# Optimization experiments

Hardware: AMD Instinct MI355X
Metric: run time of the kernel (lower is better)

## Reference

```python
import jax, jax.numpy as jnp
import numpy as np

PS = 8; STRIDE = 4; KNN = 8; POOL_RATIO = 0.5; NHEADS = 4
EPS_BN = 1e-5; EPS_LN = 1e-5


def _conv(x, w, b):
    y = jax.lax.conv_general_dilated(x, w, (1, 1), ((1, 1), (1, 1)),
                                     dimension_numbers=('NCHW', 'OIHW', 'NCHW'))
    return y + b[None, :, None, None]


def _bn_eval(x, g, b):
    # BatchNorm2d in eval mode with running_mean=0, running_var=1
    return x * (g / np.sqrt(1.0 + EPS_BN))[None, :, None, None] + b[None, :, None, None]


def _maxpool2(x):
    return jax.lax.reduce_window(x, -jnp.inf, jax.lax.max, (1, 1, 2, 2), (1, 1, 2, 2), 'VALID')


def _layernorm(x, g, b):
    m = jnp.mean(x, axis=-1, keepdims=True)
    v = jnp.var(x, axis=-1, keepdims=True)
    return (x - m) / jnp.sqrt(v + EPS_LN) * g + b


def _mha(x, in_w, in_b, out_w, out_b):
    # batched self-attention, x: (B,S,E); matches nn.MultiheadAttention eval
    B, S, E = x.shape
    hd = E // NHEADS
    qkv = x @ in_w.T + in_b                      # (B,S,3E)
    q, k, v = jnp.split(qkv, 3, axis=-1)
    def heads(t):
        return t.reshape(B, S, NHEADS, hd).transpose(0, 2, 1, 3)
    q, k, v = heads(q), heads(k), heads(v)
    att = jax.nn.softmax(jnp.einsum('bhqd,bhkd->bhqk', q, k) / np.sqrt(hd), axis=-1)
    o = jnp.einsum('bhqk,bhkd->bhqd', att, v).transpose(0, 2, 1, 3).reshape(B, S, E)
    return o @ out_w.T + out_b


def _extract_patches(feat):
    # F.unfold(feat, kernel=PS, stride=STRIDE) -> (B, N, C*PS*PS), flat order (c, ki, kj)
    B, C, H, W = feat.shape
    nph = (H - PS) // STRIDE + 1
    npw = (W - PS) // STRIDE + 1
    hi = STRIDE * jnp.arange(nph)[:, None] + jnp.arange(PS)   # (nph, PS)
    wi = STRIDE * jnp.arange(npw)[:, None] + jnp.arange(PS)   # (npw, PS)
    p = feat[:, :, hi]            # (B,C,nph,PS,W)
    p = p[:, :, :, :, wi]         # (B,C,nph,PS,npw,PS)
    p = p.transpose(0, 2, 4, 1, 3, 5).reshape(B, nph * npw, C * PS * PS)
    return p, nph, npw


def _adjacency(nph, npw):
    # positions form a deterministic grid, identical across the batch -> static adjacency
    ii, jj = np.meshgrid(np.arange(nph), np.arange(npw), indexing='ij')
    pos = np.stack([ii.ravel(), jj.ravel()], axis=1).astype(np.float32)  # (N,2)
    N = pos.shape[0]
    d = np.linalg.norm(pos[:, None, :] - pos[None, :, :], axis=-1)
    order = np.argsort(d, axis=1, kind='stable')          # ascending; col 0 is self
    tgt = order[:, 1:KNN + 1]                             # (N, KNN)
    src = np.repeat(np.arange(N), KNN)
    adj = np.zeros((N, N), dtype=np.float32)
    adj[src, tgt.ravel()] = 1.0
    adj2 = ((adj @ adj) > 0).astype(np.float32)
    np.fill_diagonal(adj2, 0.0)
    return jnp.asarray(adj), jnp.asarray(adj2)


def setup_inputs() -> dict:
    key = jax.random.key(0)
    ks = jax.random.split(key, 16)
    def lin(k, o, i):
        return jax.random.normal(k, (o, i), jnp.float32) / np.sqrt(float(i))
    B = 16
    inp = {}
    inp['x'] = jax.random.normal(ks[0], (B, 3, 256, 256), jnp.float32)
    inp['conv1_w'] = jax.random.normal(ks[1], (64, 3, 3, 3), jnp.float32) / np.sqrt(27.0)
    inp['conv1_b'] = jnp.zeros((64,), jnp.float32)
    inp['bn1_g'] = jnp.ones((64,), jnp.float32); inp['bn1_b'] = jnp.zeros((64,), jnp.float32)
    inp['conv2_w'] = jax.random.normal(ks[2], (64, 64, 3, 3), jnp.float32) / np.sqrt(576.0)
    inp['conv2_b'] = jnp.zeros((64,), jnp.float32)
    inp['bn2_g'] = jnp.ones((64,), jnp.float32); inp['bn2_b'] = jnp.zeros((64,), jnp.float32)
    inp['proj_w'] = lin(ks[3], 128, 4096); inp['proj_b'] = jnp.zeros((128,), jnp.float32)
    inp['w1_w'] = lin(ks[4], 128, 128); inp['w1_b'] = jnp.zeros((128,), jnp.float32)
    inp['w2_w'] = lin(ks[5], 128, 128); inp['w2_b'] = jnp.zeros((128,), jnp.float32)
    inp['gate_w'] = lin(ks[6], 128, 256); inp['gate_b'] = jnp.zeros((128,), jnp.float32)
    inp['score_w'] = lin(ks[7], 1, 128); inp['score_b'] = jnp.zeros((1,), jnp.float32)
    inp['in_proj_w'] = lin(ks[8], 384, 128); inp['in_proj_b'] = jnp.zeros((384,), jnp.float32)
    inp['out_proj_w'] = lin(ks[9], 128, 128); inp['out_proj_b'] = jnp.zeros((128,), jnp.float32)
    inp['ff1_w'] = lin(ks[10], 512, 128); inp['ff1_b'] = jnp.zeros((512,), jnp.float32)
    inp['ff2_w'] = lin(ks[11], 128, 512); inp['ff2_b'] = jnp.zeros((128,), jnp.float32)
    inp['ln1_g'] = jnp.ones((128,), jnp.float32); inp['ln1_b'] = jnp.zeros((128,), jnp.float32)
    inp['ln2_g'] = jnp.ones((128,), jnp.float32); inp['ln2_b'] = jnp.zeros((128,), jnp.float32)
    inp['cls1_w'] = lin(ks[12], 64, 128); inp['cls1_b'] = jnp.zeros((64,), jnp.float32)
    inp['cls2_w'] = lin(ks[13], 2, 64); inp['cls2_b'] = jnp.zeros((2,), jnp.float32)
    return inp


def reference(x, conv1_w, conv1_b, bn1_g, bn1_b, conv2_w, conv2_b, bn2_g, bn2_b,
              proj_w, proj_b, w1_w, w1_b, w2_w, w2_b, gate_w, gate_b,
              score_w, score_b, in_proj_w, in_proj_b, out_proj_w, out_proj_b,
              ff1_w, ff1_b, ff2_w, ff2_b, ln1_g, ln1_b, ln2_g, ln2_b,
              cls1_w, cls1_b, cls2_w, cls2_b):
    # backbone
    feat = _maxpool2(jax.nn.relu(_bn_eval(_conv(x, conv1_w, conv1_b), bn1_g, bn1_b)))
    feat = _maxpool2(jax.nn.relu(_bn_eval(_conv(feat, conv2_w, conv2_b), bn2_g, bn2_b)))
    # patch graph construction (edges identical for every sample)
    patches, nph, npw = _extract_patches(feat)           # (B, N, 4096)
    adj1, adj2 = _adjacency(nph, npw)                    # (N, N) binary, static
    nodes = patches @ proj_w.T + proj_b                  # (B, N, 128)
    # multi-scale aggregation: index_add over edges == adj @ x (binary adjacency)
    z1 = jnp.einsum('ij,bjd->bid', adj1, nodes) @ w1_w.T + w1_b
    z2 = jnp.einsum('ij,bjd->bid', adj2, nodes) @ w2_w.T + w2_b
    g = jax.nn.sigmoid(jnp.concatenate([z1, z2], axis=-1) @ gate_w.T + gate_b)
    z = g * z1 + (1.0 - g) * z2                          # (B, N, 128)
    # hierarchical top-k pooling
    scores = (z @ score_w.T + score_b)[..., 0]           # (B, N)
    N = scores.shape[1]
    k = max(1, int(POOL_RATIO * N))
    _, idx = jax.lax.top_k(scores, k)                    # (B, k)
    pooled = jnp.take_along_axis(z, idx[..., None], axis=1)  # (B, k, 128)
    # graph transformer layer (dropout inactive in eval)
    h = _layernorm(pooled + _mha(pooled, in_proj_w, in_proj_b, out_proj_w, out_proj_b), ln1_g, ln1_b)
    ff = jax.nn.relu(h @ ff1_w.T + ff1_b) @ ff2_w.T + ff2_b
    h = _layernorm(h + ff, ln2_g, ln2_b)
    rep = jnp.sum(h, axis=1)                             # (B, 128)
    logits = jax.nn.relu(rep @ cls1_w.T + cls1_b) @ cls2_w.T + cls2_b
    return logits
```

## Files before the change

### kernel.cpp

```cpp
#include <hip/hip_runtime.h>
#include <hip/hip_bf16.h>
#include <math.h>

typedef unsigned short u16;
typedef unsigned int   u32;
typedef unsigned long long u64;
typedef __attribute__((ext_vector_type(8))) short short8v;
typedef __attribute__((ext_vector_type(4))) float f32x4;

__device__ __forceinline__ float bf2f(u16 u) {
  union { u32 i; float f; } v; v.i = ((u32)u) << 16; return v.f;
}
__device__ __forceinline__ u16 f2bf(float f) {
  union { float f; u32 i; } v; v.f = f;
  u32 r = (v.i + 0x7FFFu + ((v.i >> 16) & 1u)) >> 16;
  return (u16)r;
}

__global__ __launch_bounds__(256, 2) void k_conv1m(
    const float* __restrict__ x,
    const u16* __restrict__ wh, const u16* __restrict__ wl,
    const float* __restrict__ cb, const float* __restrict__ g, const float* __restrict__ bb,
    u16* __restrict__ feat1, int b0)
{
  __shared__ __align__(16) float sIn[3*18*18];
  __shared__ __align__(16) u16 sAh[256*40], sAl[256*40];
  __shared__ __align__(16) u16 sBh[64*40],  sBl[64*40];
  __shared__ float sBias[64];
  const int tx = blockIdx.x, ty = blockIdx.y, bl = blockIdx.z;
  const int b = b0 + bl;
  const int y0 = ty*16, x0 = tx*16;
  const int tid = threadIdx.x;
  const int w = tid >> 6, l = tid & 63, lr = l & 15, lk = l >> 4;

  if (tid < 64) {
    float sc = g[tid] * rsqrtf(1.0f + 1e-5f);
    sBias[tid] = cb[tid] * sc + bb[tid];
  }
  {
    const int oc = tid >> 2, seg = tid & 3;
    *reinterpret_cast<uint4*>(&sBh[oc*40 + seg*8]) =
        *reinterpret_cast<const uint4*>(wh + oc*32 + seg*8);
    *reinterpret_cast<uint4*>(&sBl[oc*40 + seg*8]) =
        *reinterpret_cast<const uint4*>(wl + oc*32 + seg*8);
  }
  for (int i = tid; i < 3*18*18; i += 256) {
    const int c = i / 324, r = (i / 18) % 18, q = i % 18;
    const int yy = y0 - 1 + r, xx = x0 - 1 + q;
    float v = 0.f;
    if (yy >= 0 && yy < 256 && xx >= 0 && xx < 256)
      v = x[(((size_t)b*3 + c)*256 + yy)*256 + xx];
    sIn[i] = v;
  }
  __syncthreads();
  {
    const int py = tid >> 4, px = tid & 15;
    u32 hw[16], lw[16];
    #pragma unroll
    for (int i = 0; i < 16; i++) { hw[i] = 0u; lw[i] = 0u; }
    #pragma unroll
    for (int c = 0; c < 3; c++)
      #pragma unroll
      for (int ky = 0; ky < 3; ky++)
        #pragma unroll
        for (int kx = 0; kx < 3; kx++) {
          const int k = c*9 + ky*3 + kx;
          const float v = sIn[(c*18 + py + ky)*18 + px + kx];
          const u16 h  = f2bf(v);
          const u16 lo = f2bf(v - bf2f(h));
          hw[k >> 1] |= ((u32)h)  << ((k & 1)*16);
          lw[k >> 1] |= ((u32)lo) << ((k & 1)*16);
        }
    #pragma unroll
    for (int s = 0; s < 4; s++) {
      uint4 vh, vl;
      vh.x = hw[s*4+0]; vh.y = hw[s*4+1]; vh.z = hw[s*4+2]; vh.w = hw[s*4+3];
      vl.x = lw[s*4+0]; vl.y = lw[s*4+1]; vl.z = lw[s*4+2]; vl.w = lw[s*4+3];
      *reinterpret_cast<uint4*>(&sAh[tid*40 + s*8]) = vh;
      *reinterpret_cast<uint4*>(&sAl[tid*40 + s*8]) = vl;
    }
  }
  __syncthreads();
  f32x4 acc[4][4];
  #pragma unroll
  for (int j = 0; j < 4; j++)
    #pragma unroll
    for (int ct = 0; ct < 4; ct++)
      acc[j][ct] = (f32x4){0.f,0.f,0.f,0.f};
  #pragma unroll
  for (int j = 0; j < 4; j++) {
    const int mt = w*4 + j;
    const short8v ah = *reinterpret_cast<const short8v*>(&sAh[(mt*16 + lr)*40 + lk*8]);
    const short8v al = *reinterpret_cast<const short8v*>(&sAl[(mt*16 + lr)*40 + lk*8]);
    #pragma unroll
    for (int ct = 0; ct < 4; ct++) {
      const short8v bh = *reinterpret_cast<const short8v*>(&sBh[(ct*16 + lr)*40 + lk*8]);
      const short8v bv = *reinterpret_cast<const short8v*>(&sBl[(ct*16 + lr)*40 + lk*8]);
      acc[j][ct] = __builtin_amdgcn_mfma_f32_16x16x32_bf16(ah, bh, acc[j][ct], 0, 0, 0);
      acc[j][ct] = __builtin_amdgcn_mfma_f32_16x16x32_bf16(ah, bv, acc[j][ct], 0, 0, 0);
      acc[j][ct] = __builtin_amdgcn_mfma_f32_16x16x32_bf16(al, bh, acc[j][ct], 0, 0, 0);
      acc[j][ct] = __builtin_amdgcn_mfma_f32_16x16x32_bf16(al, bv, acc[j][ct], 0, 0, 0);
    }
  }
  #pragma unroll
  for (int j = 0; j < 2; j++) {
    const int jA = 2*j, jB = 2*j + 1;
    const int oy = ty*8 + w*2 + j;
    #pragma unroll
    for (int xh = 0; xh < 2; xh++) {
      const int ox = tx*8 + lk*2 + xh;
      #pragma unroll
      for (int ct = 0; ct < 4; ct++) {
        const int oc = ct*16 + lr;
        float m = fmaxf(fmaxf(acc[jA][ct][2*xh], acc[jA][ct][2*xh+1]),
                        fmaxf(acc[jB][ct][2*xh], acc[jB][ct][2*xh+1]));
        m = fmaxf(m + sBias[oc], 0.f);
        feat1[(((size_t)bl*128 + oy)*128 + ox)*64 + oc] = f2bf(m);
      }
    }
  }
}

__global__ __launch_bounds__(256, 2) void k_conv2m(
    const u16* __restrict__ feat1,
    const u16* __restrict__ wh, const u16* __restrict__ wl,
    const float* __restrict__ cb, const float* __restrict__ g, const float* __restrict__ bb,
    u16* __restrict__ feat2)
{
  __shared__ __align__(16) u16 sA[18*34*40];
  __shared__ __align__(16) u16 sBh[64*40], sBl[64*40];
  __shared__ float sBias[64];
  const int tx = blockIdx.x, ty = blockIdx.y, bl = blockIdx.z;
  const int y0 = ty*16, x0 = tx*32;
  const int tid = threadIdx.x;
  const int w = tid >> 6, l = tid & 63;
  const int lr = l & 15, lk = l >> 4;

  if (tid < 64) {
    float sc = g[tid] * rsqrtf(1.0f + 1e-5f);
    sBias[tid] = cb[tid] * sc + bb[tid];
  }

  f32x4 acc[8][4];
  #pragma unroll
  for (int j = 0; j < 8; j++)
    #pragma unroll
    for (int ct = 0; ct < 4; ct++)
      acc[j][ct] = (f32x4){0.f,0.f,0.f,0.f};

  for (int chunk = 0; chunk < 2; chunk++) {
    __syncthreads();
    for (int idx = tid; idx < 612*4; idx += 256) {
      const int pix = idx >> 2, seg = idx & 3;
      const int r = pix / 34, cc = pix % 34;
      const int yy = y0 - 1 + r, xx = x0 - 1 + cc;
      uint4 v = {0u,0u,0u,0u};
      if (yy >= 0 && yy < 128 && xx >= 0 && xx < 128)
        v = *reinterpret_cast<const uint4*>(
              feat1 + (((size_t)bl*128 + yy)*128 + xx)*64 + chunk*32 + seg*8);
      *reinterpret_cast<uint4*>(&sA[(size_t)(r*34 + cc)*40 + seg*8]) = v;
    }
    for (int kk = 0; kk < 9; kk++) {
      __syncthreads();
      {
        const int oc = tid >> 2, s8 = (tid & 3)*8;
        const size_t src = (size_t)(kk*2 + chunk)*2048 + tid*8;
        *reinterpret_cast<uint4*>(&sBh[oc*40 + s8]) = *reinterpret_cast<const uint4*>(wh + src);
        *reinterpret_cast<uint4*>(&sBl[oc*40 + s8]) = *reinterpret_cast<const uint4*>(wl + src);
      }
      __syncthreads();
      const int ky = kk / 3, kx = kk % 3;
      short8v a[8];
      #pragma unroll
      for (int j = 0; j < 8; j++) {
        const int m = w*8 + j;
        const int r = (m >> 1) + ky;
        const int cc = (m & 1)*16 + lr + kx;
        a[j] = *reinterpret_cast<const short8v*>(&sA[(size_t)(r*34 + cc)*40 + lk*8]);
      }
      #pragma unroll
      for (int ct = 0; ct < 4; ct++) {
        const short8v bh = *reinterpret_cast<const short8v*>(&sBh[(ct*16 + lr)*40 + lk*8]);
        const short8v bv = *reinterpret_cast<const short8v*>(&sBl[(ct*16 + lr)*40 + lk*8]);
        #pragma unroll
        for (int j = 0; j < 8; j++) {
          acc[j][ct] = __builtin_amdgcn_mfma_f32_16x16x32_bf16(a[j], bh, acc[j][ct], 0, 0, 0);
          acc[j][ct] = __builtin_amdgcn_mfma_f32_16x16x32_bf16(a[j], bv, acc[j][ct], 0, 0, 0);
        }
      }
    }
  }
  #pragma unroll
  for (int u = 0; u < 2; u++) {
    #pragma unroll
    for (int xh = 0; xh < 2; xh++) {
      const int jA = 4*u + xh, jB = 4*u + 2 + xh;
      #pragma unroll
      for (int ct = 0; ct < 4; ct++) {
        const int oc = ct*16 + lr;
        const float bias = sBias[oc];
        const float v0 = fmaxf(fmaxf(acc[jA][ct][0], acc[jA][ct][1]),
                               fmaxf(acc[jB][ct][0], acc[jB][ct][1]));
        const float v1 = fmaxf(fmaxf(acc[jA][ct][2], acc[jA][ct][3]),
                               fmaxf(acc[jB][ct][2], acc[jB][ct][3]));
        const u16 b0v = f2bf(fmaxf(v0 + bias, 0.f));
        const u16 b1v = f2bf(fmaxf(v1 + bias, 0.f));
        const int py = ty*8 + 2*w + u;
        const int px = tx*16 + xh*8 + lk*2;
        u32 pk = (u32)b0v | ((u32)b1v << 16);
        *reinterpret_cast<u32*>(&feat2[(((size_t)bl*64 + oc)*64 + py)*64 + px]) = pk;
      }
    }
  }
}

__global__ __launch_bounds__(256) void k_adj1(int* __restrict__ nbr1)
{
  __shared__ int skey[256];
  __shared__ int sred[256];
  const int i = blockIdx.x;
  const int tid = threadIdx.x;
  int key = 0x7FFFFFFF;
  if (tid < 225 && tid != i) {
    const int di = i/15 - tid/15, dj = i%15 - tid%15;
    key = (di*di + dj*dj)*256 + tid;
  }
  skey[tid] = key;
  __syncthreads();
  for (int t = 0; t < 8; t++) {
    sred[tid] = skey[tid];
    __syncthreads();
    #pragma unroll
    for (int st = 128; st > 0; st >>= 1) {
      if (tid < st) sred[tid] = min(sred[tid], sred[tid+st]);
      __syncthreads();
    }
    const int wj = sred[0] & 255;
    if (tid == 0) nbr1[i*8 + t] = wj;
    __syncthreads();
    if (tid == wj) skey[tid] = 0x7FFFFFFF;
    __syncthreads();
  }
}

__global__ __launch_bounds__(256) void k_adj2(
    const int* __restrict__ nbr1, u64* __restrict__ mask2)
{
  const int i = threadIdx.x;
  if (i >= 225) return;
  u64 m0=0, m1=0, m2=0, m3=0;
  #pragma unroll
  for (int t = 0; t < 8; t++) {
    const int tt = nbr1[i*8 + t];
    #pragma unroll
    for (int u = 0; u < 8; u++) {
      const int j = nbr1[tt*8 + u];
      const u64 bset = 1ull << (j & 63);
      const int wd = j >> 6;
      m0 |= (wd == 0) ? bset : 0ull;
      m1 |= (wd == 1) ? bset : 0ull;
      m2 |= (wd == 2) ? bset : 0ull;
      m3 |= (wd == 3) ? bset : 0ull;
    }
  }
  {
    const u64 bc = ~(1ull << (i & 63));
    const int wd = i >> 6;
    if (wd == 0) m0 &= bc; else if (wd == 1) m1 &= bc;
    else if (wd == 2) m2 &= bc; else m3 &= bc;
  }
  mask2[i*4+0] = m0; mask2[i*4+1] = m1; mask2[i*4+2] = m2; mask2[i*4+3] = m3;
}

__global__ __launch_bounds__(256) void k_prep(
    const float* __restrict__ pjw, u16* __restrict__ pwh, u16* __restrict__ pwl,
    const float* __restrict__ c2w, const float* __restrict__ bn2g,
    u16* __restrict__ wc2h, u16* __restrict__ wc2l,
    const float* __restrict__ c1w, const float* __restrict__ bn1g,
    u16* __restrict__ wc1h, u16* __restrict__ wc1l,
    const float* __restrict__ ipw, float* __restrict__ iwt,
    const float* __restrict__ opw, float* __restrict__ owt,
    const float* __restrict__ f1w, float* __restrict__ f1wt,
    const float* __restrict__ f2w, float* __restrict__ f2wt,
    const float* __restrict__ w1w, float* __restrict__ w1t,
    const float* __restrict__ w2w, float* __restrict__ w2t,
    const float* __restrict__ gw,  float* __restrict__ gwt)
{
  const int blk = blockIdx.x, tid = threadIdx.x;
  if (blk < 512) {
    const int i = (blk*256 + tid) * 4;
    float4 v = *reinterpret_cast<const float4*>(pjw + i);
    float e[4] = {v.x, v.y, v.z, v.w};
    ushort4 h, l;
    u16* hp = &h.x; u16* lp = &l.x;
    #pragma unroll
    for (int j = 0; j < 4; j++) {
      u16 hb = f2bf(e[j]);
      hp[j] = hb;
      lp[j] = f2bf(e[j] - bf2f(hb));
    }
    *reinterpret_cast<ushort4*>(pwh + i) = h;
    *reinterpret_cast<ushort4*>(pwl + i) = l;
  } else if (blk < 656) {
    const int d = (blk - 512)*256 + tid;
    if (d < 36864) {
      const int icL = d & 31, oc = (d >> 5) & 63, chunk = (d >> 11) & 1, kk = d >> 12;
      const float sc = bn2g[oc] * rsqrtf(1.0f + 1e-5f);
      const float val = c2w[((size_t)oc*64 + chunk*32 + icL)*9 + kk] * sc;
      const u16 hb = f2bf(val);
      wc2h[d] = hb;
      wc2l[d] = f2bf(val - bf2f(hb));
    }
  } else if (blk < 664) {
    const int d = (blk - 656)*256 + tid;
    if (d < 2048) {
      const int k = d & 31, oc = d >> 5;
      float val = 0.f;
      if (k < 27) val = c1w[oc*27 + k] * (bn1g[oc] * rsqrtf(1.0f + 1e-5f));
      const u16 hb = f2bf(val);
      wc1h[d] = hb;
      wc1l[d] = f2bf(val - bf2f(hb));
    }
  } else {
    const float* src; float* dst; int O, K, base;
    if      (blk <  856) { src = ipw; dst = iwt;  O = 384; K = 128; base = 664;  }
    else if (blk <  920) { src = opw; dst = owt;  O = 128; K = 128; base = 856;  }
    else if (blk < 1176) { src = f1w; dst = f1wt; O = 512; K = 128; base = 920;  }
    else if (blk < 1432) { src = f2w; dst = f2wt; O = 128; K = 512; base = 1176; }
    else if (blk < 1496) { src = w1w; dst = w1t;  O = 128; K = 128; base = 1432; }
    else if (blk < 1560) { src = w2w; dst = w2t;  O = 128; K = 128; base = 1496; }
    else                 { src = gw;  dst = gwt;  O = 128; K = 256; base = 1560; }
    const int idx = (blk - base)*256 + tid;
    if (idx < O * K) {
      const int o = idx / K, k = idx % K;
      dst[(size_t)k * O + o] = src[idx];
    }
  }
}

__global__ __launch_bounds__(256, 2) void k_projm(
    const u16* __restrict__ feat2,
    const u16* __restrict__ pwh, const u16* __restrict__ pwl,
    float* __restrict__ partial, int b0)
{
  __shared__ __align__(16) u16 sA [64][40];
  __shared__ __align__(16) u16 sBh[128][40];
  __shared__ __align__(16) u16 sBl[128][40];
  const int cx = blockIdx.x, kc = blockIdx.y, bl = blockIdx.z;
  const int b  = b0 + bl;
  const int n0 = cx * 64;
  const int rows = (225 - n0) < 64 ? (225 - n0) : 64;
  const int tid = threadIdx.x;
  const int w = tid >> 6, l = tid & 63;
  const int lr = l & 15, lk = l >> 4;

  f32x4 acc[8];
  #pragma unroll
  for (int i = 0; i < 8; i++) acc[i] = (f32x4){0.f, 0.f, 0.f, 0.f};

  const int ar = tid >> 2, aci = tid & 3;
  const int an = n0 + ar;
  const int aph = an / 15, apw = an % 15;
  const int kbeg = kc * 512, kend = kbeg + 512;

  uint4 pA, pBh[2], pBl[2];
  auto loadstep = [&](int k0) {
    const int c  = k0 >> 6;
    const int i0 = (k0 & 63) >> 3;
    uint2 g0 = {0u,0u}, g1 = {0u,0u};
    if (ar < rows) {
      const u16* src = feat2 + (((size_t)bl*64 + c)*64 + aph*4 + i0 + aci)*64 + apw*4;
      g0 = *reinterpret_cast<const uint2*>(src);
      g1 = *reinterpret_cast<const uint2*>(src + 4);
    }
    pA.x = g0.x; pA.y = g0.y; pA.z = g1.x; pA.w = g1.y;
    #pragma unroll
    for (int p = 0; p < 2; p++) {
      const int idx = p*256 + tid;
      const int col = idx >> 2, seg = idx & 3;
      const size_t off = (size_t)col*4096 + k0 + seg*8;
      pBh[p] = *reinterpret_cast<const uint4*>(pwh + off);
      pBl[p] = *reinterpret_cast<const uint4*>(pwl + off);
    }
  };

  loadstep(kbeg);
  for (int k0 = kbeg; k0 < kend; k0 += 32) {
    __syncthreads();
    *reinterpret_cast<uint4*>(&sA[ar][aci*8]) = pA;
    #pragma unroll
    for (int p = 0; p < 2; p++) {
      const int idx = p*256 + tid;
      const int col = idx >> 2, seg = idx & 3;
      *reinterpret_cast<uint4*>(&sBh[col][seg*8]) = pBh[p];
      *reinterpret_cast<uint4*>(&sBl[col][seg*8]) = pBl[p];
    }
    __syncthreads();
    if (k0 + 32 < kend) loadstep(k0 + 32);
    short8v a = *reinterpret_cast<const short8v*>(&sA[w*16 + lr][lk*8]);
    #pragma unroll
    for (int ct = 0; ct < 8; ct++) {
      short8v bh = *reinterpret_cast<const short8v*>(&sBh[ct*16 + lr][lk*8]);
      short8v bv = *reinterpret_cast<const short8v*>(&sBl[ct*16 + lr][lk*8]);
      acc[ct] = __builtin_amdgcn_mfma_f32_16x16x32_bf16(a, bh, acc[ct], 0, 0, 0);
      acc[ct] = __builtin_amdgcn_mfma_f32_16x16x32_bf16(a, bv, acc[ct], 0, 0, 0);
    }
  }
  #pragma unroll
  for (int ct = 0; ct < 8; ct++) {
    const int col = ct*16 + lr;
    #pragma unroll
    for (int v = 0; v < 4; v++) {
      const int r = w*16 + lk*4 + v;
      if (r < rows)
        partial[(((size_t)kc*16 + b)*225 + n0 + r)*128 + col] = acc[ct][v];
    }
  }
}

__global__ __launch_bounds__(128) void k_projr(
    const float* __restrict__ partial, const float* __restrict__ pb,
    float* __restrict__ nodes, int b0)
{
  const int n = blockIdx.x, bl = blockIdx.y;
  const int b = b0 + bl;
  const int d = threadIdx.x;
  float s = pb[d];
  #pragma unroll
  for (int kc = 0; kc < 8; kc++)
    s += partial[(((size_t)kc*16 + b)*225 + n)*128 + d];
  nodes[((size_t)b*225 + n)*128 + d] = s;
}

__global__ __launch_bounds__(128) void k_agg(
    const float* __restrict__ nodes, const int* __restrict__ nbr1,
    const u64* __restrict__ mask2,
    float* __restrict__ a1buf, float* __restrict__ a2buf)
{
  const int n = blockIdx.x, b = blockIdx.y;
  const int d = threadIdx.x;
  const float* nb = nodes + (size_t)b * 225 * 128;
  float a1 = 0.f;
  #pragma unroll
  for (int t = 0; t < 8; t++) a1 += nb[(size_t)nbr1[n*8+t]*128 + d];
  float a2 = 0.f;
  for (int wd = 0; wd < 4; wd++) {
    u64 m = mask2[n*4 + wd];
    while (m) {
      int j = wd*64 + __builtin_ctzll(m);
      a2 += nb[(size_t)j*128 + d];
      m &= m - 1;
    }
  }
  a1buf[((size_t)b*225 + n)*128 + d] = a1;
  a2buf[((size_t)b*225 + n)*128 + d] = a2;
}

__global__ __launch_bounds__(256) void k_gz(
    const float* __restrict__ a1buf, const float* __restrict__ a2buf,
    const float* __restrict__ w1t, const float* __restrict__ w1b,
    const float* __restrict__ w2t, const float* __restrict__ w2b,
    const float* __restrict__ gwt, const float* __restrict__ gb,
    const float* __restrict__ sw, const float* __restrict__ sb,
    float* __restrict__ zbuf, float* __restrict__ scores)
{
  __shared__ float sA1[2][128], sA2[2][128], sC[2][256], sRed[2][128];
  const int row0 = blockIdx.x * 2;
  const int tid = threadIdx.x;
  const int d = tid & 127, rr = tid >> 7;
  const int row = row0 + rr;
  sA1[rr][d] = a1buf[(size_t)row*128 + d];
  sA2[rr][d] = a2buf[(size_t)row*128 + d];
  __syncthreads();
  float z1 = w1b[d], z2 = w2b[d];
  #pragma unroll 4
  for (int k = 0; k < 128; k++) {
    z1 += w1t[k*128 + d] * sA1[rr][k];
    z2 += w2t[k*128 + d] * sA2[rr][k];
  }
  sC[rr][d] = z1; sC[rr][128 + d] = z2;
  __syncthreads();
  float gl = gb[d];
  #pragma unroll 4
  for (int k = 0; k < 256; k++)
    gl += gwt[k*128 + d] * sC[rr][k];
  const float gg = 1.f / (1.f + expf(-gl));
  const float zv = gg * z1 + (1.f - gg) * z2;
  zbuf[(size_t)row*128 + d] = zv;
  sRed[rr][d] = zv * sw[d];
  __syncthreads();
  if (tid < 32) {
    const int r = tid >> 4, j = tid & 15;
    float part = 0.f;
    #pragma unroll
    for (int i = 0; i < 8; i++) part += sRed[r][j*8 + i];
    #pragma unroll
    for (int m = 8; m >= 1; m >>= 1) part += __shfl_xor(part, m, 64);
    if (j == 0) scores[row0 + r] = part + sb[0];
  }
}

__global__ __launch_bounds__(256) void k_topk(
    const float* __restrict__ scores, int* __restrict__ sel)
{
  __shared__ float ss[225];
  const int b = blockIdx.x, tid = threadIdx.x;
  if (tid < 112) sel[b*112 + tid] = tid;
  if (tid < 225) ss[tid] = scores[b*225 + tid];
  __syncthreads();
  if (tid < 225) {
    float s = ss[tid];
    int rank = 0;
    for (int j = 0; j < 225; j++) {
      float sj = ss[j];
      rank += (sj > s) || (sj == s && j < tid);
    }
    if (rank < 112) sel[b*112 + rank] = tid;
  }
}

__global__ __launch_bounds__(256) void k_qkv(
    const float* __restrict__ zbuf, const int* __restrict__ sel,
    const float* __restrict__ iwt, const float* __restrict__ ib,
    float* __restrict__ q, float* __restrict__ k, float* __restrict__ v)
{
  __shared__ float sx[14][128];
  const int s0 = blockIdx.x * 14, b = blockIdx.y;
  const int tid = threadIdx.x;
  const int c = tid & 127, half = tid >> 7;
  const int r0 = half * 7;

  for (int idx = tid; idx < 14*128; idx += 256) {
    const int r = idx >> 7, dd = idx & 127;
    int row = sel[b*112 + s0 + r];
    row = row < 0 ? 0 : (row > 224 ? 224 : row);
    sx[r][dd] = zbuf[((size_t)b*225 + row)*128 + dd];
  }
  __syncthreads();

  float acc[3][7];
  #pragma unroll
  for (int p = 0; p < 3; p++)
    #pragma unroll
    for (int rr = 0; rr < 7; rr++) acc[p][rr] = ib[p*128 + c];
  for (int kk = 0; kk < 128; kk++) {
    float wv[3];
    #pragma unroll
    for (int p = 0; p < 3; p++) wv[p] = iwt[kk*384 + p*128 + c];
    #pragma unroll
    for (int rr = 0; rr < 7; rr++) {
      const float xv = sx[r0 + rr][kk];
      #pragma unroll
      for (int p = 0; p < 3; p++) acc[p][rr] += wv[p] * xv;
    }
  }
  const int h = c >> 5, t = c & 31;
  float* outs[3] = {q, k, v};
  #pragma unroll
  for (int p = 0; p < 3; p++)
    #pragma unroll
    for (int rr = 0; rr < 7; rr++)
      outs[p][(((size_t)b*4 + h)*112 + s0 + r0 + rr)*32 + t] = acc[p][rr];
}

__global__ __launch_bounds__(256) void k_attn(
    const float* __restrict__ q, const float* __restrict__ k,
    const float* __restrict__ v, float* __restrict__ o)
{
  __shared__ float sK[112*33], sV[112*33];
  __shared__ float sQ[14*33];
  __shared__ float sP[14][112];
  const int qc = blockIdx.x, h = blockIdx.y, b = blockIdx.z;
  const size_t base = ((size_t)b*4 + h) * 112 * 32;
  const int tid = threadIdx.x;
  for (int i = tid; i < 112*32; i += 256) {
    const int r = i >> 5, c = i & 31;
    sK[r*33 + c] = k[base + i];
    sV[r*33 + c] = v[base + i];
  }
  for (int i = tid; i < 14*32; i += 256) {
    const int r = i >> 5, c = i & 31;
    sQ[r*33 + c] = q[base + (size_t)(qc*14)*32 + i];
  }
  __syncthreads();
  const int qg = tid >> 4, j = tid & 15;
  if (qg < 14) {
    const float scale = 0.17677669529663687f;
    float pv[7];
    float mx = -INFINITY;
    #pragma unroll
    for (int t7 = 0; t7 < 7; t7++) {
      const int kk = j + t7*16;
      float s = 0.f;
      #pragma unroll
      for (int t = 0; t < 32; t++) s += sQ[qg*33 + t] * sK[kk*33 + t];
      pv[t7] = s * scale;
      mx = fmaxf(mx, pv[t7]);
    }
    #pragma unroll
    for (int m = 8; m >= 1; m >>= 1) mx = fmaxf(mx, __shfl_xor(mx, m, 16));
    float lsum = 0.f;
    #pragma unroll
    for (int t7 = 0; t7 < 7; t7++) { pv[t7] = expf(pv[t7] - mx); lsum += pv[t7]; }
    #pragma unroll
    for (int m = 8; m >= 1; m >>= 1) lsum += __shfl_xor(lsum, m, 16);
    const float inv = 1.f / lsum;
    #pragma unroll
    for (int t7 = 0; t7 < 7; t7++) sP[qg][j + t7*16] = pv[t7] * inv;
  }
  __syncthreads();
  if (qg < 14) {
    const int s = qc*14 + qg;
    float o0 = 0.f, o1 = 0.f;
    for (int kk = 0; kk < 112; kk++) {
      const float p = sP[qg][kk];
      o0 += p * sV[kk*33 + j];
      o1 += p * sV[kk*33 + j + 16];
    }
    float* op = o + ((size_t)b*112 + s)*128 + h*32;
    op[j] = o0;
    op[j + 16] = o1;
  }
}

__global__ __launch_bounds__(256) void k_oln(
    const float* __restrict__ o, const float* __restrict__ zbuf,
    const int* __restrict__ sel,
    const float* __restrict__ owt, const float* __restrict__ ob,
    const float* __restrict__ lg, const float* __restrict__ lb,
    float* __restrict__ h1)
{
  __shared__ float sO[14][128], sV[14][128];
  __shared__ float sMean[14], sRstd[14];
  const int s0 = blockIdx.x * 14, b = blockIdx.y;
  const int tid = threadIdx.x;
  const int d = tid & 127, half = tid >> 7;
  const int r0 = half * 7;

  for (int idx = tid; idx < 14*128; idx += 256) {
    const int r = idx >> 7, dd = idx & 127;
    sO[r][dd] = o[((size_t)b*112 + s0 + r)*128 + dd];
  }
  __syncthreads();

  float acc[7];
  #pragma unroll
  for (int rr = 0; rr < 7; rr++) acc[rr] = ob[d];
  for (int kk = 0; kk < 128; kk++) {
    const float wv = owt[kk*128 + d];
    #pragma unroll
    for (int rr = 0; rr < 7; rr++) acc[rr] += wv * sO[r0 + rr][kk];
  }
  #pragma unroll
  for (int rr = 0; rr < 7; rr++) {
    int row = sel[b*112 + s0 + r0 + rr];
    row = row < 0 ? 0 : (row > 224 ? 224 : row);
    acc[rr] += zbuf[((size_t)b*225 + row)*128 + d];
    sV[r0 + rr][d] = acc[rr];
  }
  __syncthreads();
  {
    const int r = tid >> 4, j = tid & 15;
    if (r < 14) {
      float p1 = 0.f, p2 = 0.f;
      #pragma unroll
      for (int i = 0; i < 8; i++) { float v = sV[r][j*8 + i]; p1 += v; p2 += v*v; }
      #pragma unroll
      for (int m = 8; m >= 1; m >>= 1) {
        p1 += __shfl_xor(p1, m, 64);
        p2 += __shfl_xor(p2, m, 64);
      }
      if (j == 0) {
        const float mean = p1 * (1.f/128.f);
        sMean[r] = mean;
        sRstd[r] = rsqrtf(p2 * (1.f/128.f) - mean*mean + 1e-5f);
      }
    }
  }
  __syncthreads();
  for (int idx = tid; idx < 14*128; idx += 256) {
    const int r = idx >> 7, dd = idx & 127;
    h1[((size_t)b*112 + s0 + r)*128 + dd] =
        (sV[r][dd] - sMean[r]) * sRstd[r] * lg[dd] + lb[dd];
  }
}

__global__ __launch_bounds__(256) void k_ffn(
    const float* __restrict__ h1,
    const float* __restrict__ f1wt, const float* __restrict__ f1b,
    const float* __restrict__ f2wt, const float* __restrict__ f2b,
    const float* __restrict__ lg, const float* __restrict__ lb,
    float* __restrict__ h2)
{
  __shared__ float sh[14][128];
  __shared__ float sf[14][512];
  __shared__ float sV[14][128];
  __shared__ float sMean[14], sRstd[14];
  const int s0 = blockIdx.x * 14, b = blockIdx.y;
  const int tid = threadIdx.x;
  const int d = tid & 127, half = tid >> 7;
  const int r0 = half * 7;

  for (int idx = tid; idx < 14*128; idx += 256) {
    const int r = idx >> 7, dd = idx & 127;
    sh[r][dd] = h1[((size_t)b*112 + s0 + r)*128 + dd];
  }
  __syncthreads();
  {
    float a0[14], a1[14];
    const float b0 = f1b[tid], b1 = f1b[tid + 256];
    #pragma unroll
    for (int r = 0; r < 14; r++) { a0[r] = b0; a1[r] = b1; }
    for (int kk = 0; kk < 128; kk++) {
      const float w0 = f1wt[kk*512 + tid];
      const float w1 = f1wt[kk*512 + tid + 256];
      #pragma unroll
      for (int r = 0; r < 14; r++) {
        const float xv = sh[r][kk];
        a0[r] += w0 * xv;
        a1[r] += w1 * xv;
      }
    }
    #pragma unroll
    for (int r = 0; r < 14; r++) {
      sf[r][tid]       = fmaxf(a0[r], 0.f);
      sf[r][tid + 256] = fmaxf(a1[r], 0.f);
    }
  }
  __syncthreads();
  {
    float acc[7];
    #pragma unroll
    for (int rr = 0; rr < 7; rr++) acc[rr] = f2b[d];
    for (int kk = 0; kk < 512; kk++) {
      const float wv = f2wt[kk*128 + d];
      #pragma unroll
      for (int rr = 0; rr < 7; rr++) acc[rr] += wv * sf[r0 + rr][kk];
    }
    #pragma unroll
    for (int rr = 0; rr < 7; rr++)
      sV[r0 + rr][d] = sh[r0 + rr][d] + acc[rr];
  }
  __syncthreads();
  {
    const int r = tid >> 4, j = tid & 15;
    if (r < 14) {
      float p1 = 0.f, p2 = 0.f;
      #pragma unroll
      for (int i = 0; i < 8; i++) { float v = sV[r][j*8 + i]; p1 += v; p2 += v*v; }
      #pragma unroll
      for (int m = 8; m >= 1; m >>= 1) {
        p1 += __shfl_xor(p1, m, 64);
        p2 += __shfl_xor(p2, m, 64);
      }
      if (j == 0) {
        const float mean = p1 * (1.f/128.f);
        sMean[r] = mean;
        sRstd[r] = rsqrtf(p2 * (1.f/128.f) - mean*mean + 1e-5f);
      }
    }
  }
  __syncthreads();
  for (int idx = tid; idx < 14*128; idx += 256) {
    const int r = idx >> 7, dd = idx & 127;
    h2[((size_t)b*112 + s0 + r)*128 + dd] =
        (sV[r][dd] - sMean[r]) * sRstd[r] * lg[dd] + lb[dd];
  }
}

__global__ __launch_bounds__(64) void k_cls(
    const float* __restrict__ h2,
    const float* __restrict__ c1w, const float* __restrict__ c1b,
    const float* __restrict__ c2w, const float* __restrict__ c2b,
    float* __restrict__ out)
{
  __shared__ float sr[128], sc[64];
  const int b = blockIdx.x, tid = threadIdx.x;
  float r0 = 0.f, r1 = 0.f;
  for (int s2 = 0; s2 < 112; s2++) {
    const float* row = h2 + ((size_t)b*112 + s2)*128;
    r0 += row[tid];
    r1 += row[tid + 64];
  }
  sr[tid] = r0; sr[tid + 64] = r1;
  __syncthreads();
  float acc = c1b[tid];
  const float* wr = c1w + (size_t)tid * 128;
  for (int kk = 0; kk < 128; kk++) acc += wr[kk] * sr[kk];
  sc[tid] = fmaxf(acc, 0.f);
  __syncthreads();
  if (tid < 2) {
    float l = c2b[tid];
    for (int kk = 0; kk < 64; kk++) l += c2w[tid*64 + kk] * sc[kk];
    out[b*2 + tid] = l;
  }
}

extern "C" void kernel_launch(void* const* d_in, const int* in_sizes, int n_in,
                              void* d_out, int out_size, void* d_ws, size_t ws_size,
                              hipStream_t stream)
{
  const float* x    = (const float*)d_in[0];
  const float* c1w  = (const float*)d_in[1];
  const float* c1b  = (const float*)d_in[2];
  const float* bn1g = (const float*)d_in[3];
  const float* bn1b = (const float*)d_in[4];
  const float* c2w  = (const float*)d_in[5];
  const float* c2b  = (const float*)d_in[6];
  const float* bn2g = (const float*)d_in[7];
  const float* bn2b = (const float*)d_in[8];
  const float* pjw  = (const float*)d_in[9];
  const float* pjb  = (const float*)d_in[10];
  const float* w1w  = (const float*)d_in[11];
  const float* w1b  = (const float*)d_in[12];
  const float* w2w  = (const float*)d_in[13];
  const float* w2b  = (const float*)d_in[14];
  const float* gw   = (const float*)d_in[15];
  const float* gb   = (const float*)d_in[16];
  const float* scw  = (const float*)d_in[17];
  const float* scb  = (const float*)d_in[18];
  const float* ipw  = (const float*)d_in[19];
  const float* ipb  = (const float*)d_in[20];
  const float* opw  = (const float*)d_in[21];
  const float* opb  = (const float*)d_in[22];
  const float* f1w  = (const float*)d_in[23];
  const float* f1b  = (const float*)d_in[24];
  const float* f2w  = (const float*)d_in[25];
  const float* f2b  = (const float*)d_in[26];
  const float* l1g  = (const float*)d_in[27];
  const float* l1b  = (const float*)d_in[28];
  const float* l2g  = (const float*)d_in[29];
  const float* l2b  = (const float*)d_in[30];
  const float* cl1w = (const float*)d_in[31];
  const float* cl1b = (const float*)d_in[32];
  const float* cl2w = (const float*)d_in[33];
  const float* cl2b = (const float*)d_in[34];

  char* p = (char*)d_ws;
  auto alloc = [&](size_t n) { char* r = p; p += (n + 255) & ~(size_t)255; return r; };
  u64*   mask2  = (u64*)  alloc(900    * sizeof(u64));
  int*   nbr1   = (int*)  alloc(1800   * sizeof(int));
  int*   sel    = (int*)  alloc(1792   * sizeof(int));
  float* scores = (float*)alloc(3600   * sizeof(float));
  u16*   pwh    = (u16*)  alloc(524288 * sizeof(u16));
  u16*   pwl    = (u16*)  alloc(524288 * sizeof(u16));
  u16*   wc2h   = (u16*)  alloc(36864  * sizeof(u16));
  u16*   wc2l   = (u16*)  alloc(36864  * sizeof(u16));
  u16*   wc1h   = (u16*)  alloc(2048   * sizeof(u16));
  u16*   wc1l   = (u16*)  alloc(2048   * sizeof(u16));
  float* iwt    = (float*)alloc(49152  * sizeof(float));
  float* owt    = (float*)alloc(16384  * sizeof(float));
  float* f1wt   = (float*)alloc(65536  * sizeof(float));
  float* f2wt   = (float*)alloc(65536  * sizeof(float));
  float* w1t    = (float*)alloc(16384  * sizeof(float));
  float* w2t    = (float*)alloc(16384  * sizeof(float));
  float* gwt    = (float*)alloc(32768  * sizeof(float));
  float* partial= (float*)alloc(8ull*16*225*128 * sizeof(float));
  float* a1buf  = (float*)alloc(460800 * sizeof(float));
  float* a2buf  = (float*)alloc(460800 * sizeof(float));
  float* zbuf   = (float*)alloc(460800 * sizeof(float));
  float* nodes  = (float*)alloc(460800 * sizeof(float));
  const size_t fixed_bytes = (size_t)(p - (char*)d_ws);

  const size_t qkv_bytes = 3ull * 229376ull * sizeof(float);
  const size_t per_batch = 64ull*128*128*2 + 64ull*64*64*2;
  int BC = 16;
  size_t s3 = 0;
  for (;; BC >>= 1) {
    s3 = (size_t)BC * per_batch; if (s3 < qkv_bytes) s3 = qkv_bytes;
    if (fixed_bytes + s3 + 65536 <= ws_size) break;
    if (BC == 1) { return; }
  }
  char* S3 = alloc(s3);

  u16*   feat1 = (u16*)S3;
  u16*   feat2 = (u16*)(S3 + (size_t)BC * 2097152ull);
  float* qb    = (float*)S3;
  float* kb    = qb + 229376;
  float* vb    = kb + 229376;
  float* obuf  = nodes;
  float* hbuf  = nodes + 229376;

  k_adj1<<<225, 256, 0, stream>>>(nbr1);
  k_adj2<<<1, 256, 0, stream>>>(nbr1, mask2);
  k_prep<<<1688, 256, 0, stream>>>(pjw, pwh, pwl, c2w, bn2g, wc2h, wc2l,
                                   c1w, bn1g, wc1h, wc1l,
                                   ipw, iwt, opw, owt, f1w, f1wt, f2w, f2wt,
                                   w1w, w1t, w2w, w2t, gw, gwt);

  for (int b0 = 0; b0 < 16; b0 += BC) {
    k_conv1m<<<dim3(16,16,BC), 256, 0, stream>>>(x, wc1h, wc1l, c1b, bn1g, bn1b, feat1, b0);
    k_conv2m<<<dim3(4,8,BC), 256, 0, stream>>>(feat1, wc2h, wc2l, c2b, bn2g, bn2b, feat2);
    k_projm <<<dim3(4,8,BC), 256, 0, stream>>>(feat2, pwh, pwl, partial, b0);
    k_projr <<<dim3(225,BC), 128, 0, stream>>>(partial, pjb, nodes, b0);
  }

  k_agg  <<<dim3(225,16), 128, 0, stream>>>(nodes, nbr1, mask2, a1buf, a2buf);
  k_gz   <<<1800, 256, 0, stream>>>(a1buf, a2buf, w1t, w1b, w2t, w2b,
                                    gwt, gb, scw, scb, zbuf, scores);
  k_topk <<<16, 256, 0, stream>>>(scores, sel);
  k_qkv  <<<dim3(8,16), 256, 0, stream>>>(zbuf, sel, iwt, ipb, qb, kb, vb);
  k_attn <<<dim3(8,4,16), 256, 0, stream>>>(qb, kb, vb, obuf);
  k_oln  <<<dim3(8,16), 256, 0, stream>>>(obuf, zbuf, sel, owt, opb, l1g, l1b, hbuf);
  k_ffn  <<<dim3(8,16), 256, 0, stream>>>(hbuf, f1wt, f1b, f2wt, f2b, l2g, l2b, hbuf);
  k_cls  <<<16, 64, 0, stream>>>(hbuf, cl1w, cl1b, cl2w, cl2b, (float*)d_out);
}
```

Baseline: 288.0 us.

## Double-buffer weight tiles in conv2 and proj GEMMs, drop low-low conv1 MFMA term

In conv2 and the patch projection kernel, weight tiles are now loaded into registers one step ahead and stored into a second LDS buffer, which halves the barriers per k-step and overlaps global loads with MFMA work. The projection kernel also stops staging the patch A-operand in LDS and reads it straight from global memory into registers per lane. Separately, conv1 drops the low-times-low product in its split-bf16 emulation, cutting its MFMA count by a quarter at a small accuracy cost. The extra LDS buffer raises shared-memory use, and the direct global A loads in proj may be less coalesced.

```diff
diff --git a/kernel.cpp b/kernel.cpp
--- a/kernel.cpp
+++ b/kernel.cpp
@@ -99,7 +99,6 @@
       acc[j][ct] = __builtin_amdgcn_mfma_f32_16x16x32_bf16(ah, bh, acc[j][ct], 0, 0, 0);
       acc[j][ct] = __builtin_amdgcn_mfma_f32_16x16x32_bf16(ah, bv, acc[j][ct], 0, 0, 0);
       acc[j][ct] = __builtin_amdgcn_mfma_f32_16x16x32_bf16(al, bh, acc[j][ct], 0, 0, 0);
-      acc[j][ct] = __builtin_amdgcn_mfma_f32_16x16x32_bf16(al, bv, acc[j][ct], 0, 0, 0);
     }
   }
   #pragma unroll
@@ -128,7 +127,7 @@
     u16* __restrict__ feat2)
 {
   __shared__ __align__(16) u16 sA[18*34*40];
-  __shared__ __align__(16) u16 sBh[64*40], sBl[64*40];
+  __shared__ __align__(16) u16 sBh[2][64*40], sBl[2][64*40];
   __shared__ float sBias[64];
   const int tx = blockIdx.x, ty = blockIdx.y, bl = blockIdx.z;
   const int y0 = ty*16, x0 = tx*32;
@@ -148,8 +147,21 @@
     for (int ct = 0; ct < 4; ct++)
       acc[j][ct] = (f32x4){0.f,0.f,0.f,0.f};
 
+  const int ocB = tid >> 2, s8B = (tid & 3)*8;
+  uint4 rBh, rBl;
+  auto ldB = [&](int chunk, int kk) {
+    const size_t src = (size_t)(kk*2 + chunk)*2048 + tid*8;
+    rBh = *reinterpret_cast<const uint4*>(wh + src);
+    rBl = *reinterpret_cast<const uint4*>(wl + src);
+  };
+  auto stB = [&](int buf) {
+    *reinterpret_cast<uint4*>(&sBh[buf][ocB*40 + s8B]) = rBh;
+    *reinterpret_cast<uint4*>(&sBl[buf][ocB*40 + s8B]) = rBl;
+  };
+
   for (int chunk = 0; chunk < 2; chunk++) {
     __syncthreads();
+    ldB(chunk, 0);
     for (int idx = tid; idx < 612*4; idx += 256) {
       const int pix = idx >> 2, seg = idx & 3;
       const int r = pix / 34, cc = pix % 34;
@@ -160,15 +172,11 @@
               feat1 + (((size_t)bl*128 + yy)*128 + xx)*64 + chunk*32 + seg*8);
       *reinterpret_cast<uint4*>(&sA[(size_t)(r*34 + cc)*40 + seg*8]) = v;
     }
+    stB(0);
+    __syncthreads();
+    int cur = 0;
     for (int kk = 0; kk < 9; kk++) {
-      __syncthreads();
-      {
-        const int oc = tid >> 2, s8 = (tid & 3)*8;
-        const size_t src = (size_t)(kk*2 + chunk)*2048 + tid*8;
-        *reinterpret_cast<uint4*>(&sBh[oc*40 + s8]) = *reinterpret_cast<const uint4*>(wh + src);
-        *reinterpret_cast<uint4*>(&sBl[oc*40 + s8]) = *reinterpret_cast<const uint4*>(wl + src);
-      }
-      __syncthreads();
+      if (kk + 1 < 9) ldB(chunk, kk + 1);
       const int ky = kk / 3, kx = kk % 3;
       short8v a[8];
       #pragma unroll
@@ -180,13 +188,18 @@
       }
       #pragma unroll
       for (int ct = 0; ct < 4; ct++) {
-        const short8v bh = *reinterpret_cast<const short8v*>(&sBh[(ct*16 + lr)*40 + lk*8]);
-        const short8v bv = *reinterpret_cast<const short8v*>(&sBl[(ct*16 + lr)*40 + lk*8]);
+        const short8v bh = *reinterpret_cast<const short8v*>(&sBh[cur][(ct*16 + lr)*40 + lk*8]);
+        const short8v bv = *reinterpret_cast<const short8v*>(&sBl[cur][(ct*16 + lr)*40 + lk*8]);
         #pragma unroll
         for (int j = 0; j < 8; j++) {
           acc[j][ct] = __builtin_amdgcn_mfma_f32_16x16x32_bf16(a[j], bh, acc[j][ct], 0, 0, 0);
           acc[j][ct] = __builtin_amdgcn_mfma_f32_16x16x32_bf16(a[j], bv, acc[j][ct], 0, 0, 0);
         }
+      }
+      if (kk + 1 < 9) {
+        stB(cur ^ 1);
+        __syncthreads();
+        cur ^= 1;
       }
     }
   }
@@ -343,9 +356,8 @@
     const u16* __restrict__ pwh, const u16* __restrict__ pwl,
     float* __restrict__ partial, int b0)
 {
-  __shared__ __align__(16) u16 sA [64][40];
-  __shared__ __align__(16) u16 sBh[128][40];
-  __shared__ __align__(16) u16 sBl[128][40];
+  __shared__ __align__(16) u16 sBh[2][128*40];
+  __shared__ __align__(16) u16 sBl[2][128*40];
   const int cx = blockIdx.x, kc = blockIdx.y, bl = blockIdx.z;
   const int b  = b0 + bl;
   const int n0 = cx * 64;
@@ -358,52 +370,55 @@
   #pragma unroll
   for (int i = 0; i < 8; i++) acc[i] = (f32x4){0.f, 0.f, 0.f, 0.f};
 
-  const int ar = tid >> 2, aci = tid & 3;
-  const int an = n0 + ar;
+  int an = n0 + w*16 + lr;
+  if (an > 224) an = 224;
   const int aph = an / 15, apw = an % 15;
   const int kbeg = kc * 512, kend = kbeg + 512;
 
-  uint4 pA, pBh[2], pBl[2];
-  auto loadstep = [&](int k0) {
-    const int c  = k0 >> 6;
-    const int i0 = (k0 & 63) >> 3;
-    uint2 g0 = {0u,0u}, g1 = {0u,0u};
-    if (ar < rows) {
-      const u16* src = feat2 + (((size_t)bl*64 + c)*64 + aph*4 + i0 + aci)*64 + apw*4;
-      g0 = *reinterpret_cast<const uint2*>(src);
-      g1 = *reinterpret_cast<const uint2*>(src + 4);
-    }
-    pA.x = g0.x; pA.y = g0.y; pA.z = g1.x; pA.w = g1.y;
+  uint4 rBh[2], rBl[2];
+  auto ldB = [&](int k0) {
     #pragma unroll
     for (int p = 0; p < 2; p++) {
       const int idx = p*256 + tid;
       const int col = idx >> 2, seg = idx & 3;
       const size_t off = (size_t)col*4096 + k0 + seg*8;
-      pBh[p] = *reinterpret_cast<const uint4*>(pwh + off);
-      pBl[p] = *reinterpret_cast<const uint4*>(pwl + off);
+      rBh[p] = *reinterpret_cast<const uint4*>(pwh + off);
+      rBl[p] = *reinterpret_cast<const uint4*>(pwl + off);
     }
   };
-
-  loadstep(kbeg);
-  for (int k0 = kbeg; k0 < kend; k0 += 32) {
-    __syncthreads();
-    *reinterpret_cast<uint4*>(&sA[ar][aci*8]) = pA;
+  auto stB = [&](int buf) {
     #pragma unroll
     for (int p = 0; p < 2; p++) {
       const int idx = p*256 + tid;
       const int col = idx >> 2, seg = idx & 3;
-      *reinterpret_cast<uint4*>(&sBh[col][seg*8]) = pBh[p];
-      *reinterpret_cast<uint4*>(&sBl[col][seg*8]) = pBl[p];
-    }
-    __syncthreads();
-    if (k0 + 32 < kend) loadstep(k0 + 32);
-    short8v a = *reinterpret_cast<const short8v*>(&sA[w*16 + lr][lk*8]);
+      *reinterpret_cast<uint4*>(&sBh[buf][col*40 + seg*8]) = rBh[p];
+      *reinterpret_cast<uint4*>(&sBl[buf][col*40 + seg*8]) = rBl[p];
+    }
+  };
+
+  ldB(kbeg);
+  stB(0);
+  __syncthreads();
+  int cur = 0;
+  for (int k0 = kbeg; k0 < kend; k0 += 32) {
+    if (k0 + 32 < kend) ldB(k0 + 32);
+    const int c = k0 >> 6;
+    const int i = ((k0 & 32) >> 3) + lk;
+    const u16* ap = feat2 + (((size_t)bl*64 + c)*64 + aph*4 + i)*64 + apw*4;
+    union { short8v v; uint2 u[2]; } a;
+    a.u[0] = *reinterpret_cast<const uint2*>(ap);
+    a.u[1] = *reinterpret_cast<const uint2*>(ap + 4);
     #pragma unroll
     for (int ct = 0; ct < 8; ct++) {
-      short8v bh = *reinterpret_cast<const short8v*>(&sBh[ct*16 + lr][lk*8]);
-      short8v bv = *reinterpret_cast<const short8v*>(&sBl[ct*16 + lr][lk*8]);
-      acc[ct] = __builtin_amdgcn_mfma_f32_16x16x32_bf16(a, bh, acc[ct], 0, 0, 0);
-      acc[ct] = __builtin_amdgcn_mfma_f32_16x16x32_bf16(a, bv, acc[ct], 0, 0, 0);
+      const short8v bh = *reinterpret_cast<const short8v*>(&sBh[cur][(ct*16 + lr)*40 + lk*8]);
+      const short8v bv = *reinterpret_cast<const short8v*>(&sBl[cur][(ct*16 + lr)*40 + lk*8]);
+      acc[ct] = __builtin_amdgcn_mfma_f32_16x16x32_bf16(a.v, bh, acc[ct], 0, 0, 0);
+      acc[ct] = __builtin_amdgcn_mfma_f32_16x16x32_bf16(a.v, bv, acc[ct], 0, 0, 0);
+    }
+    if (k0 + 32 < kend) {
+      stB(cur ^ 1);
+      __syncthreads();
+      cur ^= 1;
     }
   }
   #pragma unroll
```

Result: no change. 288.8 us (+0.3%).
